# Optimization experiments

Measured on AMD Instinct MI355X. Metric: run time of the kernel, lower is better.

## Reference

```python
import jax, jax.numpy as jnp
import numpy as np

MAX_STEPS = 8
EPS = 0.1
LAM = 5.0


def setup_inputs() -> dict:
    key = jax.random.key(0)
    k1, k2, k3, k4, k5 = jax.random.split(key, 5)
    n0 = m0 = 192
    E = 191  # tree edges ~ n0 - 1
    return {
        "E1f": jax.random.randint(k1, (E, 2), 0, n0),
        "E1b": jax.random.randint(k2, (E, 2), 0, n0),
        "E2f": jax.random.randint(k3, (E, 2), 0, n0),  # unused by forward (kept for signature parity)
        "cost": jax.random.uniform(k4, (n0, m0), dtype=jnp.float32),
        "constr_f": jax.random.uniform(k5, (m0, m0), dtype=jnp.float32),
    }


def reference(E1f, E1b, E2f, cost, constr_f):
    n0, m0 = cost.shape
    S = n0 + m0
    # pad cost -> [S, S], constr_f -> [S, S] (right cols zero then bottom rows one)
    cost_p = jnp.pad(cost, ((0, m0), (0, n0)))
    cf = jnp.pad(constr_f, ((0, 0), (0, n0)))
    cf = jnp.pad(cf, ((0, n0), (0, 0)), constant_values=1.0)

    phi = cost_p.T                          # [S, S]
    phie = phi / EPS
    psi_f = (LAM * (1.0 - cf))[:, :, None]  # [S, S, 1]
    psi_b = jnp.transpose(psi_f, (1, 0, 2))

    # cdist(dst, arange(S)) == 0 indicator is exactly a one-hot of the dst index
    to_f = jax.nn.one_hot(E1f[:, 1], S, dtype=phi.dtype)  # [E, S]
    to_b = jax.nn.one_hot(E1b[:, 1], S, dtype=phi.dtype)  # [E, S]
    E = to_f.shape[0]

    def step(carry, _):
        u, v, msg_f, msg_b, sum_f, sum_b = carry
        base = sum_f + sum_b - phie
        u = jax.nn.logsumexp(base - v, axis=-2, keepdims=True)  # [1, S]
        v = jax.nn.logsumexp(base - u, axis=-1, keepdims=True)  # [S, 1]
        A = phie + u + v - sum_f - sum_b                        # [S, S]
        term_f = A @ to_f.T                                     # [S, E]
        lse_f = jax.nn.logsumexp(-(psi_f / EPS + msg_b[:, None, :]), axis=0)  # [S, E]
        msg_f = 0.5 * (msg_f + term_f + lse_f)
        sum_f = msg_f @ to_f                                    # [S, S]
        A2 = phie + u + v - sum_f - sum_b
        term_b = A2 @ to_b.T
        lse_b = jax.nn.logsumexp(-(psi_b / EPS + msg_f[:, None, :]), axis=0)
        msg_b = 0.5 * (msg_b + term_b + lse_b)
        sum_b = msg_b @ to_b
        return (u, v, msg_f, msg_b, sum_f, sum_b), None

    f32 = phi.dtype
    init = (
        jnp.zeros((1, S), f32), jnp.zeros((S, 1), f32),
        jnp.zeros((S, E), f32), jnp.zeros((S, E), f32),
        jnp.zeros((S, S), f32), jnp.zeros((S, S), f32),
    )
    (u, v, _, _, sum_f, sum_b), _ = jax.lax.scan(step, init, None, length=MAX_STEPS)

    logp = jnp.minimum(sum_f + sum_b - phie - u - v, 0.0)
    return jnp.exp(logp).T
```

## Files before the change

kernel.cpp:

```cpp
#include <hip/hip_runtime.h>
#include <math.h>

#define S      384
#define N0     192
#define NE     191
#define MAXADJ 16
#define E50    1.9287498e-22f

#define OFF_W     0
#define OFF_WT    36864
#define OFF_PHIE  73728
#define OFF_MSGF  147456
#define OFF_MSGB  221184
#define OFF_MXF   294912
#define OFF_MXB   368640
#define OFF_SBT   442368
#define OFF_BASET 516096
#define OFF_U     589824
#define OFF_V     590016
#define OFF_MAXF  590400
#define OFF_MAXB  590592
#define OFF_HIF   590784
#define OFF_LOF   590976
#define OFF_HIB   591168
#define OFF_LOB   591360
#define OFF_UHI   591552
#define OFF_INT   591616
#define IOFF_DSTF 0
#define IOFF_DSTB 192
#define IOFF_CNTF 384
#define IOFF_CNTB 576
#define IOFF_ADJF 768
#define IOFF_ADJB (768 + 192*MAXADJ)

__global__ __launch_bounds__(256) void k_setup(
    const int* __restrict__ E1f, const int* __restrict__ E1b,
    const float* __restrict__ cost, const float* __restrict__ constr,
    float* __restrict__ ws)
{
    int tid = blockIdx.x * 256 + threadIdx.x;
    int nt  = gridDim.x * 256;

    for (int idx = tid; idx < 192 * 192; idx += nt) {
        int k = idx / 192, s = idx % 192;
        float w = __expf(-50.f * (1.f - constr[idx]));
        ws[OFF_W + idx] = w;
        ws[OFF_WT + s * 192 + k] = w;
    }
    for (int idx = tid; idx < 192 * S; idx += nt) {
        int j = idx / S, i = idx % S;
        ws[OFF_PHIE + idx] = (i < N0) ? -10.f * cost[j * N0 + i] : 0.f;
        ws[OFF_MSGF + idx] = 0.f;
        ws[OFF_MSGB + idx] = 0.f;
        ws[OFF_MXF + idx]  = 0.f;
        ws[OFF_MXB + idx]  = (j < NE) ? 1.f : 0.f;
    }
    for (int i = tid; i < S; i += nt) ws[OFF_V + i] = 0.f;
    for (int i = tid; i < 192; i += nt) {
        ws[OFF_U + i] = 0.f;
        ws[OFF_MAXF + i] = 0.f; ws[OFF_MAXB + i] = 0.f;
        ws[OFF_HIF + i] = 0.f;  ws[OFF_LOF + i] = 0.f;
        ws[OFF_HIB + i] = (i < NE) ? 192.f : 0.f;
        ws[OFF_LOB + i] = (i < NE) ? 192.f : 0.f;
    }
    if (tid == 0) ws[OFF_UHI] = 0.f;

    int* ip = (int*)(ws + OFF_INT);
    for (int e = tid; e < 192; e += nt) {
        ip[IOFF_DSTF + e] = (e < NE) ? E1f[2 * e + 1] : 0;
        ip[IOFF_DSTB + e] = (e < NE) ? E1b[2 * e + 1] : 0;
    }
    for (int b = tid; b < 192; b += nt) {
        int cf = 0, cb = 0;
        for (int e = 0; e < NE; ++e) {
            if (E1f[2 * e + 1] == b && cf < MAXADJ) ip[IOFF_ADJF + b * MAXADJ + cf++] = e;
            if (E1b[2 * e + 1] == b && cb < MAXADJ) ip[IOFF_ADJB + b * MAXADJ + cb++] = e;
        }
        ip[IOFF_CNTF + b] = cf;
        ip[IOFF_CNTB + b] = cb;
    }
}

__global__ __launch_bounds__(256) void k_uv1(float* __restrict__ ws)
{
    int bid = blockIdx.x, t = threadIdx.x;
    int l = t & 63, w = t >> 6;
    const float* V = ws + OFF_V;

    if (bid == 48) {
        if (w == 0) {
            float m = -1e30f, x[6];
#pragma unroll
            for (int q = 0; q < 6; ++q) { x[q] = -V[l + 64 * q]; m = fmaxf(m, x[q]); }
#pragma unroll
            for (int o = 32; o; o >>= 1) m = fmaxf(m, __shfl_xor(m, o, 64));
            float sm = 0.f;
#pragma unroll
            for (int q = 0; q < 6; ++q) sm += __expf(x[q] - m);
#pragma unroll
            for (int o = 32; o; o >>= 1) sm += __shfl_xor(sm, o, 64);
            if (l == 0) ws[OFF_UHI] = m + __logf(sm);
        }
        return;
    }

    int j = bid * 4 + w;
    const int* ip = (const int*)(ws + OFF_INT);
    int cF = ip[IOFF_CNTF + j], cB = ip[IOFF_CNTB + j];
    const int* aF = ip + IOFF_ADJF + j * MAXADJ;
    const int* aB = ip + IOFF_ADJB + j * MAXADJ;

    float sft[6] = {0,0,0,0,0,0}, sbt[6] = {0,0,0,0,0,0};
    for (int q = 0; q < cF; ++q) {
        const float* mr = ws + OFF_MSGF + aF[q] * S;
#pragma unroll
        for (int p = 0; p < 6; ++p) sft[p] += mr[l + 64 * p];
    }
    for (int q = 0; q < cB; ++q) {
        const float* mr = ws + OFF_MSGB + aB[q] * S;
#pragma unroll
        for (int p = 0; p < 6; ++p) sbt[p] += mr[l + 64 * p];
    }

    float x[6], m = -1e30f;
#pragma unroll
    for (int p = 0; p < 6; ++p) {
        int i = l + 64 * p;
        float bt = ws[OFF_PHIE + j * S + i] + sft[p] + sbt[p];
        ws[OFF_BASET + j * S + i] = bt;
        ws[OFF_SBT + j * S + i]   = sbt[p];
        x[p] = bt - V[i];
        m = fmaxf(m, x[p]);
    }
#pragma unroll
    for (int o = 32; o; o >>= 1) m = fmaxf(m, __shfl_xor(m, o, 64));
    float sm = 0.f;
#pragma unroll
    for (int p = 0; p < 6; ++p) sm += __expf(x[p] - m);
#pragma unroll
    for (int o = 32; o; o >>= 1) sm += __shfl_xor(sm, o, 64);
    if (l == 0) ws[OFF_U + j] = m + __logf(sm);
}

__global__ __launch_bounds__(256) void k_v(float* __restrict__ ws)
{
    __shared__ float Ul[192];
    __shared__ float msh[16][17], ssh[16][17];
    int t = threadIdx.x, bid = blockIdx.x;
    if (t < 192) Ul[t] = ws[OFF_U + t];
    __syncthreads();

    const float* BT = ws + OFF_BASET;
    int il = t & 15, jg = t >> 4;
    int i = bid * 16 + il;

    float m = -1e30f, sm = 0.f;
#pragma unroll 4
    for (int j = jg; j < 192; j += 16) {
        float x = BT[j * S + i] - Ul[j];
        float mn = fmaxf(m, x);
        sm = sm * __expf(m - mn) + __expf(x - mn);
        m = mn;
    }
    msh[jg][il] = m; ssh[jg][il] = sm;
    __syncthreads();

    if (jg == 0) {
        float M = msh[0][il], Ss = ssh[0][il];
#pragma unroll
        for (int g = 1; g < 16; ++g) {
            float m2 = msh[g][il], s2 = ssh[g][il];
            float mn = fmaxf(M, m2);
            Ss = Ss * __expf(M - mn) + s2 * __expf(m2 - mn);
            M = mn;
        }
        float xt = __logf(192.f) - ws[OFF_UHI];
        float mn = fmaxf(M, xt);
        Ss = Ss * __expf(M - mn) + __expf(xt - mn);
        ws[OFF_V + i] = mn + __logf(Ss);
    }
}

__global__ __launch_bounds__(256) void k_msg(float* __restrict__ ws, int fwd)
{
    __shared__ float mx[192];
    __shared__ float red[256], red2[256];
    int e = blockIdx.x, t = threadIdx.x;
    const int* ip = (const int*)(ws + OFF_INT);

    float* MSG  = ws + (fwd ? OFF_MSGF : OFF_MSGB);
    float* MX   = ws + (fwd ? OFF_MXF  : OFF_MXB);
    const float* MXin = ws + (fwd ? OFF_MXB : OFF_MXF);
    const float* Wm   = ws + (fwd ? OFF_W   : OFF_WT);

    float mPrev = fwd ? ws[OFF_MAXB + e] : ws[OFF_MAXF + e];
    float hi    = fwd ? ws[OFF_HIB + e]  : ws[OFF_HIF + e];
    float lo    = fwd ? ws[OFF_LOB + e]  : ws[OFF_LOF + e];
    float addLo = fwd ? hi : E50 * hi;
    float yHi   = fwd ? (hi + E50 * lo) : (lo + hi);
    float lyHi  = __logf(yHi);

    int d = fwd ? ip[IOFF_DSTF + e] : ip[IOFF_DSTB + e];
    float uD = ws[OFF_U + d];
    const float* V = ws + OFF_V;

    if (t < 192) mx[t] = MXin[e * S + t];
    __syncthreads();

    float acc = 0.f;
    if (t < 192) {
#pragma unroll 8
        for (int k = 0; k < 192; ++k)
            acc += Wm[k * 192 + t] * mx[k];
    }

    int s1 = t, s2 = t + 256;
    float bt1, bt2 = 0.f;
    if (fwd) {
        bt1 = ws[OFF_BASET + d * S + s1];
        if (s2 < S) bt2 = ws[OFF_BASET + d * S + s2];
    } else {
        int cF = ip[IOFF_CNTF + d];
        const int* aF = ip + IOFF_ADJF + d * MAXADJ;
        bt1 = ws[OFF_PHIE + d * S + s1] + ws[OFF_SBT + d * S + s1];
        if (s2 < S) bt2 = ws[OFF_PHIE + d * S + s2] + ws[OFF_SBT + d * S + s2];
        for (int q = 0; q < cF; ++q) {
            const float* mr = ws + OFF_MSGF + aF[q] * S;
            bt1 += mr[s1];
            if (s2 < S) bt2 += mr[s2];
        }
    }

    float logy1 = (s1 < 192) ? __logf(acc + addLo) : lyHi;
    float x1 = 0.5f * (MSG[e * S + s1] + uD + V[s1] - bt1 + mPrev + logy1);
    float x2 = 1e30f;
    if (s2 < S) {
        x2 = 0.5f * (MSG[e * S + s2] + uD + V[s2] - bt2 + mPrev + lyHi);
        MSG[e * S + s2] = x2;
    }
    MSG[e * S + s1] = x1;

    red[t] = fminf(x1, x2);
    __syncthreads();
    for (int o = 128; o; o >>= 1) {
        if (t < o) red[t] = fminf(red[t], red[t + o]);
        __syncthreads();
    }
    float mn = red[0];
    __syncthreads();

    float mx1 = __expf(mn - x1);
    float mx2 = (s2 < S) ? __expf(mn - x2) : 0.f;
    MX[e * S + s1] = mx1;
    if (s2 < S) MX[e * S + s2] = mx2;
    if (t == 0) {
        if (fwd) ws[OFF_MAXF + e] = -mn; else ws[OFF_MAXB + e] = -mn;
    }

    red[t]  = (t < 192) ? mx1 : 0.f;
    red2[t] = ((t >= 192) ? mx1 : 0.f) + mx2;
    __syncthreads();
    for (int o = 128; o; o >>= 1) {
        if (t < o) { red[t] += red[t + o]; red2[t] += red2[t + o]; }
        __syncthreads();
    }
    if (t == 0) {
        if (fwd) { ws[OFF_LOF + e] = red[0]; ws[OFF_HIF + e] = red2[0]; }
        else     { ws[OFF_LOB + e] = red[0]; ws[OFF_HIB + e] = red2[0]; }
    }
}

__global__ __launch_bounds__(256) void k_final(const float* __restrict__ ws,
                                               float* __restrict__ out)
{
    int t = threadIdx.x;
    const int* ip = (const int*)(ws + OFF_INT);
    const float* V = ws + OFF_V;
    float uhi = ws[OFF_UHI];

    for (int a = blockIdx.x * 6; a < blockIdx.x * 6 + 6; ++a) {
        if (a < 192) {
            float ua = ws[OFF_U + a];
            int cF = ip[IOFF_CNTF + a], cB = ip[IOFF_CNTB + a];
            const int* aF = ip + IOFF_ADJF + a * MAXADJ;
            const int* aB = ip + IOFF_ADJB + a * MAXADJ;
            for (int b = t; b < S; b += 256) {
                float bt = ws[OFF_PHIE + a * S + b];
                for (int q = 0; q < cF; ++q) bt += ws[OFF_MSGF + aF[q] * S + b];
                for (int q = 0; q < cB; ++q) bt += ws[OFF_MSGB + aB[q] * S + b];
                out[a * S + b] = __expf(fminf(bt - ua - V[b], 0.f));
            }
        } else {
            for (int b = t; b < S; b += 256)
                out[a * S + b] = __expf(fminf(-uhi - V[b], 0.f));
        }
    }
}

extern "C" void kernel_launch(void* const* d_in, const int* in_sizes, int n_in,
                              void* d_out, int out_size, void* d_ws, size_t ws_size,
                              hipStream_t stream)
{
    const int*   E1f    = (const int*)d_in[0];
    const int*   E1b    = (const int*)d_in[1];
    const float* cost   = (const float*)d_in[3];
    const float* constr = (const float*)d_in[4];

    float* ws = (float*)d_ws;

    k_setup<<<64, 256, 0, stream>>>(E1f, E1b, cost, constr, ws);

    for (int step = 0; step < 8; ++step) {
        k_uv1<<<49, 256, 0, stream>>>(ws);
        k_v<<<24, 256, 0, stream>>>(ws);
        k_msg<<<NE, 256, 0, stream>>>(ws, 1);
        k_msg<<<NE, 256, 0, stream>>>(ws, 0);
    }

    k_final<<<64, 256, 0, stream>>>(ws, (float*)d_out);
}
```

Before: 250.3 us.

## Fuse all iteration kernels into one persistent cooperative kernel with counter sync

Replaces the 32 per-step kernel launches plus the final kernel with one cooperative persistent kernel of 264 blocks. Blocks take fixed roles (u rows, v columns, per-edge messages) and synchronise through global atomic counters with spin-waits instead of kernel boundaries. The aim is to remove launch and drain overhead, which dominates because each stage does very little work. The cost is relaxed atomic loads and stores at agent scope, spin-waiting, and the risk of memory-ordering bugs, since there are no explicit fences.

```diff
diff --git a/kernel.cpp b/kernel.cpp
--- a/kernel.cpp
+++ b/kernel.cpp
@@ -32,6 +32,30 @@
 #define IOFF_CNTB 576
 #define IOFF_ADJF 768
 #define IOFF_ADJB (768 + 192*MAXADJ)
+#define IOFF_SYNC (768 + 2*192*MAXADJ)
+
+#define AGT __HIP_MEMORY_SCOPE_AGENT
+
+__device__ __forceinline__ float ldc(const float* p) {
+    return __hip_atomic_load(p, __ATOMIC_RELAXED, AGT);
+}
+__device__ __forceinline__ void stc(float* p, float v) {
+    __hip_atomic_store(p, v, __ATOMIC_RELAXED, AGT);
+}
+
+__device__ __forceinline__ void arrive(unsigned* c) {
+    asm volatile("s_waitcnt vmcnt(0)" ::: "memory");
+    __syncthreads();
+    if (threadIdx.x == 0)
+        __hip_atomic_fetch_add(c, 1u, __ATOMIC_RELAXED, AGT);
+}
+__device__ __forceinline__ void wait_cnt(unsigned* c, unsigned tgt) {
+    if (threadIdx.x == 0) {
+        while (__hip_atomic_load(c, __ATOMIC_RELAXED, AGT) < tgt)
+            __builtin_amdgcn_s_sleep(2);
+    }
+    __syncthreads();
+}
 
 __global__ __launch_bounds__(256) void k_setup(
     const int* __restrict__ E1f, const int* __restrict__ E1b,
@@ -54,6 +78,8 @@
         ws[OFF_MSGB + idx] = 0.f;
         ws[OFF_MXF + idx]  = 0.f;
         ws[OFF_MXB + idx]  = (j < NE) ? 1.f : 0.f;
+        ws[OFF_SBT + idx]  = 0.f;
+        ws[OFF_BASET + idx] = 0.f;
     }
     for (int i = tid; i < S; i += nt) ws[OFF_V + i] = 0.f;
     for (int i = tid; i < 192; i += nt) {
@@ -79,220 +105,238 @@
         ip[IOFF_CNTF + b] = cf;
         ip[IOFF_CNTB + b] = cb;
     }
-}
-
-__global__ __launch_bounds__(256) void k_uv1(float* __restrict__ ws)
+    unsigned* sc = (unsigned*)(ip + IOFF_SYNC);
+    for (int i = tid; i < 32; i += nt) sc[i] = 0u;
+}
+
+__global__ __launch_bounds__(256) void k_iter(float* __restrict__ ws,
+                                              float* __restrict__ out)
 {
-    int bid = blockIdx.x, t = threadIdx.x;
-    int l = t & 63, w = t >> 6;
-    const float* V = ws + OFF_V;
-
-    if (bid == 48) {
-        if (w == 0) {
-            float m = -1e30f, x[6];
-#pragma unroll
-            for (int q = 0; q < 6; ++q) { x[q] = -V[l + 64 * q]; m = fmaxf(m, x[q]); }
-#pragma unroll
-            for (int o = 32; o; o >>= 1) m = fmaxf(m, __shfl_xor(m, o, 64));
-            float sm = 0.f;
-#pragma unroll
-            for (int q = 0; q < 6; ++q) sm += __expf(x[q] - m);
-#pragma unroll
-            for (int o = 32; o; o >>= 1) sm += __shfl_xor(sm, o, 64);
-            if (l == 0) ws[OFF_UHI] = m + __logf(sm);
+    const int bid = blockIdx.x, t = threadIdx.x;
+    const int l = t & 63, w = t >> 6;
+    int* ip = (int*)(ws + OFF_INT);
+    unsigned* sync = (unsigned*)(ip + IOFF_SYNC);
+
+    __shared__ float mx[192];
+    __shared__ float Ul[192];
+    __shared__ float red[256], red2[256];
+    __shared__ float msh[16][17], ssh[16][17];
+
+    for (int step = 0; step < 8; ++step) {
+        unsigned* sc = sync + step * 4;
+
+        if (bid < 49) {
+            if (step > 0) wait_cnt(sync + (step - 1) * 4 + 3, NE);
+            if (bid == 48) {
+                if (w == 0) {
+                    float m = -1e30f, x[6];
+#pragma unroll
+                    for (int q = 0; q < 6; ++q) {
+                        x[q] = -ldc(ws + OFF_V + l + 64 * q);
+                        m = fmaxf(m, x[q]);
+                    }
+#pragma unroll
+                    for (int o = 32; o; o >>= 1) m = fmaxf(m, __shfl_xor(m, o, 64));
+                    float sm = 0.f;
+#pragma unroll
+                    for (int q = 0; q < 6; ++q) sm += __expf(x[q] - m);
+#pragma unroll
+                    for (int o = 32; o; o >>= 1) sm += __shfl_xor(sm, o, 64);
+                    if (l == 0) stc(ws + OFF_UHI, m + __logf(sm));
+                }
+            } else {
+                int j = bid * 4 + w;
+                int cF = ip[IOFF_CNTF + j], cB = ip[IOFF_CNTB + j];
+                const int* aF = ip + IOFF_ADJF + j * MAXADJ;
+                const int* aB = ip + IOFF_ADJB + j * MAXADJ;
+
+                float sft[6] = {0,0,0,0,0,0}, sbt[6] = {0,0,0,0,0,0};
+                for (int q = 0; q < cF; ++q) {
+                    const float* mr = ws + OFF_MSGF + aF[q] * S;
+#pragma unroll
+                    for (int p = 0; p < 6; ++p) sft[p] += ldc(mr + l + 64 * p);
+                }
+                for (int q = 0; q < cB; ++q) {
+                    const float* mr = ws + OFF_MSGB + aB[q] * S;
+#pragma unroll
+                    for (int p = 0; p < 6; ++p) sbt[p] += ldc(mr + l + 64 * p);
+                }
+
+                float x[6], m = -1e30f;
+#pragma unroll
+                for (int p = 0; p < 6; ++p) {
+                    int i = l + 64 * p;
+                    float bt = ws[OFF_PHIE + j * S + i] + sft[p] + sbt[p];
+                    stc(ws + OFF_BASET + j * S + i, bt);
+                    stc(ws + OFF_SBT + j * S + i, sbt[p]);
+                    x[p] = bt - ldc(ws + OFF_V + i);
+                    m = fmaxf(m, x[p]);
+                }
+#pragma unroll
+                for (int o = 32; o; o >>= 1) m = fmaxf(m, __shfl_xor(m, o, 64));
+                float sm = 0.f;
+#pragma unroll
+                for (int p = 0; p < 6; ++p) sm += __expf(x[p] - m);
+#pragma unroll
+                for (int o = 32; o; o >>= 1) sm += __shfl_xor(sm, o, 64);
+                if (l == 0) stc(ws + OFF_U + j, m + __logf(sm));
+            }
+            arrive(&sc[0]);
+        } else if (bid < 73) {
+            wait_cnt(&sc[0], 49u);
+            if (t < 192) Ul[t] = ldc(ws + OFF_U + t);
+            __syncthreads();
+
+            int il = t & 15, jg = t >> 4;
+            int i = (bid - 49) * 16 + il;
+
+            float m = -1e30f, sm = 0.f;
+            for (int j = jg; j < 192; j += 16) {
+                float x = ldc(ws + OFF_BASET + j * S + i) - Ul[j];
+                float mn = fmaxf(m, x);
+                sm = sm * __expf(m - mn) + __expf(x - mn);
+                m = mn;
+            }
+            msh[jg][il] = m; ssh[jg][il] = sm;
+            __syncthreads();
+
+            if (jg == 0) {
+                float M = msh[0][il], Ss = ssh[0][il];
+#pragma unroll
+                for (int g = 1; g < 16; ++g) {
+                    float m2 = msh[g][il], s2 = ssh[g][il];
+                    float mn = fmaxf(M, m2);
+                    Ss = Ss * __expf(M - mn) + s2 * __expf(m2 - mn);
+                    M = mn;
+                }
+                float xt = __logf(192.f) - ldc(ws + OFF_UHI);
+                float mn = fmaxf(M, xt);
+                Ss = Ss * __expf(M - mn) + __expf(xt - mn);
+                stc(ws + OFF_V + i, mn + __logf(Ss));
+            }
+            arrive(&sc[1]);
+        } else {
+            int e = bid - 73;
+            for (int fwd = 1; fwd >= 0; --fwd) {
+                wait_cnt(fwd ? &sc[1] : &sc[2], fwd ? 24u : (unsigned)NE);
+
+                float* MSG  = ws + (fwd ? OFF_MSGF : OFF_MSGB);
+                float* MX   = ws + (fwd ? OFF_MXF  : OFF_MXB);
+                const float* MXin = ws + (fwd ? OFF_MXB : OFF_MXF);
+                const float* Wm   = ws + (fwd ? OFF_W   : OFF_WT);
+
+                float mPrev = fwd ? ws[OFF_MAXB + e] : ws[OFF_MAXF + e];
+                float hi    = fwd ? ws[OFF_HIB + e]  : ws[OFF_HIF + e];
+                float lo    = fwd ? ws[OFF_LOB + e]  : ws[OFF_LOF + e];
+                float addLo = fwd ? hi : E50 * hi;
+                float yHi   = fwd ? (hi + E50 * lo) : (lo + hi);
+                float lyHi  = __logf(yHi);
+
+                int d = fwd ? ip[IOFF_DSTF + e] : ip[IOFF_DSTB + e];
+                float uD = ldc(ws + OFF_U + d);
+
+                if (t < 192) mx[t] = MXin[e * S + t];
+                __syncthreads();
+
+                float acc = 0.f;
+                if (t < 192) {
+#pragma unroll 8
+                    for (int k = 0; k < 192; ++k)
+                        acc += Wm[k * 192 + t] * mx[k];
+                }
+
+                int s1 = t, s2 = t + 256;
+                float bt1, bt2 = 0.f;
+                if (fwd) {
+                    bt1 = ldc(ws + OFF_BASET + d * S + s1);
+                    if (s2 < S) bt2 = ldc(ws + OFF_BASET + d * S + s2);
+                } else {
+                    int cF = ip[IOFF_CNTF + d];
+                    const int* aF = ip + IOFF_ADJF + d * MAXADJ;
+                    bt1 = ws[OFF_PHIE + d * S + s1] + ldc(ws + OFF_SBT + d * S + s1);
+                    if (s2 < S)
+                        bt2 = ws[OFF_PHIE + d * S + s2] + ldc(ws + OFF_SBT + d * S + s2);
+                    for (int q = 0; q < cF; ++q) {
+                        const float* mr = ws + OFF_MSGF + aF[q] * S;
+                        bt1 += ldc(mr + s1);
+                        if (s2 < S) bt2 += ldc(mr + s2);
+                    }
+                }
+
+                float v1 = ldc(ws + OFF_V + s1);
+                float v2 = (s2 < S) ? ldc(ws + OFF_V + s2) : 0.f;
+
+                float logy1 = (s1 < 192) ? __logf(acc + addLo) : lyHi;
+                float x1 = 0.5f * (ldc(MSG + e * S + s1) + uD + v1 - bt1 + mPrev + logy1);
+                float x2 = 1e30f;
+                if (s2 < S) {
+                    x2 = 0.5f * (ldc(MSG + e * S + s2) + uD + v2 - bt2 + mPrev + lyHi);
+                    stc(MSG + e * S + s2, x2);
+                }
+                stc(MSG + e * S + s1, x1);
+
+                red[t] = fminf(x1, x2);
+                __syncthreads();
+                for (int o = 128; o; o >>= 1) {
+                    if (t < o) red[t] = fminf(red[t], red[t + o]);
+                    __syncthreads();
+                }
+                float mn = red[0];
+                __syncthreads();
+
+                float mx1 = __expf(mn - x1);
+                float mx2 = (s2 < S) ? __expf(mn - x2) : 0.f;
+                MX[e * S + s1] = mx1;
+                if (s2 < S) MX[e * S + s2] = mx2;
+                if (t == 0) {
+                    if (fwd) ws[OFF_MAXF + e] = -mn; else ws[OFF_MAXB + e] = -mn;
+                }
+
+                red[t]  = (t < 192) ? mx1 : 0.f;
+                red2[t] = ((t >= 192) ? mx1 : 0.f) + mx2;
+                __syncthreads();
+                for (int o = 128; o; o >>= 1) {
+                    if (t < o) { red[t] += red[t + o]; red2[t] += red2[t + o]; }
+                    __syncthreads();
+                }
+                if (t == 0) {
+                    if (fwd) { ws[OFF_LOF + e] = red[0]; ws[OFF_HIF + e] = red2[0]; }
+                    else     { ws[OFF_LOB + e] = red[0]; ws[OFF_HIB + e] = red2[0]; }
+                }
+                __syncthreads();
+                arrive(fwd ? &sc[2] : &sc[3]);
+            }
         }
-        return;
-    }
-
-    int j = bid * 4 + w;
-    const int* ip = (const int*)(ws + OFF_INT);
-    int cF = ip[IOFF_CNTF + j], cB = ip[IOFF_CNTB + j];
-    const int* aF = ip + IOFF_ADJF + j * MAXADJ;
-    const int* aB = ip + IOFF_ADJB + j * MAXADJ;
-
-    float sft[6] = {0,0,0,0,0,0}, sbt[6] = {0,0,0,0,0,0};
-    for (int q = 0; q < cF; ++q) {
-        const float* mr = ws + OFF_MSGF + aF[q] * S;
-#pragma unroll
-        for (int p = 0; p < 6; ++p) sft[p] += mr[l + 64 * p];
-    }
-    for (int q = 0; q < cB; ++q) {
-        const float* mr = ws + OFF_MSGB + aB[q] * S;
-#pragma unroll
-        for (int p = 0; p < 6; ++p) sbt[p] += mr[l + 64 * p];
-    }
-
-    float x[6], m = -1e30f;
-#pragma unroll
-    for (int p = 0; p < 6; ++p) {
-        int i = l + 64 * p;
-        float bt = ws[OFF_PHIE + j * S + i] + sft[p] + sbt[p];
-        ws[OFF_BASET + j * S + i] = bt;
-        ws[OFF_SBT + j * S + i]   = sbt[p];
-        x[p] = bt - V[i];
-        m = fmaxf(m, x[p]);
-    }
-#pragma unroll
-    for (int o = 32; o; o >>= 1) m = fmaxf(m, __shfl_xor(m, o, 64));
-    float sm = 0.f;
-#pragma unroll
-    for (int p = 0; p < 6; ++p) sm += __expf(x[p] - m);
-#pragma unroll
-    for (int o = 32; o; o >>= 1) sm += __shfl_xor(sm, o, 64);
-    if (l == 0) ws[OFF_U + j] = m + __logf(sm);
-}
-
-__global__ __launch_bounds__(256) void k_v(float* __restrict__ ws)
-{
-    __shared__ float Ul[192];
-    __shared__ float msh[16][17], ssh[16][17];
-    int t = threadIdx.x, bid = blockIdx.x;
-    if (t < 192) Ul[t] = ws[OFF_U + t];
-    __syncthreads();
-
-    const float* BT = ws + OFF_BASET;
-    int il = t & 15, jg = t >> 4;
-    int i = bid * 16 + il;
-
-    float m = -1e30f, sm = 0.f;
-#pragma unroll 4
-    for (int j = jg; j < 192; j += 16) {
-        float x = BT[j * S + i] - Ul[j];
-        float mn = fmaxf(m, x);
-        sm = sm * __expf(m - mn) + __expf(x - mn);
-        m = mn;
-    }
-    msh[jg][il] = m; ssh[jg][il] = sm;
-    __syncthreads();
-
-    if (jg == 0) {
-        float M = msh[0][il], Ss = ssh[0][il];
-#pragma unroll
-        for (int g = 1; g < 16; ++g) {
-            float m2 = msh[g][il], s2 = ssh[g][il];
-            float mn = fmaxf(M, m2);
-            Ss = Ss * __expf(M - mn) + s2 * __expf(m2 - mn);
-            M = mn;
-        }
-        float xt = __logf(192.f) - ws[OFF_UHI];
-        float mn = fmaxf(M, xt);
-        Ss = Ss * __expf(M - mn) + __expf(xt - mn);
-        ws[OFF_V + i] = mn + __logf(Ss);
-    }
-}
-
-__global__ __launch_bounds__(256) void k_msg(float* __restrict__ ws, int fwd)
-{
-    __shared__ float mx[192];
-    __shared__ float red[256], red2[256];
-    int e = blockIdx.x, t = threadIdx.x;
-    const int* ip = (const int*)(ws + OFF_INT);
-
-    float* MSG  = ws + (fwd ? OFF_MSGF : OFF_MSGB);
-    float* MX   = ws + (fwd ? OFF_MXF  : OFF_MXB);
-    const float* MXin = ws + (fwd ? OFF_MXB : OFF_MXF);
-    const float* Wm   = ws + (fwd ? OFF_W   : OFF_WT);
-
-    float mPrev = fwd ? ws[OFF_MAXB + e] : ws[OFF_MAXF + e];
-    float hi    = fwd ? ws[OFF_HIB + e]  : ws[OFF_HIF + e];
-    float lo    = fwd ? ws[OFF_LOB + e]  : ws[OFF_LOF + e];
-    float addLo = fwd ? hi : E50 * hi;
-    float yHi   = fwd ? (hi + E50 * lo) : (lo + hi);
-    float lyHi  = __logf(yHi);
-
-    int d = fwd ? ip[IOFF_DSTF + e] : ip[IOFF_DSTB + e];
-    float uD = ws[OFF_U + d];
-    const float* V = ws + OFF_V;
-
-    if (t < 192) mx[t] = MXin[e * S + t];
-    __syncthreads();
-
-    float acc = 0.f;
-    if (t < 192) {
-#pragma unroll 8
-        for (int k = 0; k < 192; ++k)
-            acc += Wm[k * 192 + t] * mx[k];
-    }
-
-    int s1 = t, s2 = t + 256;
-    float bt1, bt2 = 0.f;
-    if (fwd) {
-        bt1 = ws[OFF_BASET + d * S + s1];
-        if (s2 < S) bt2 = ws[OFF_BASET + d * S + s2];
-    } else {
-        int cF = ip[IOFF_CNTF + d];
-        const int* aF = ip + IOFF_ADJF + d * MAXADJ;
-        bt1 = ws[OFF_PHIE + d * S + s1] + ws[OFF_SBT + d * S + s1];
-        if (s2 < S) bt2 = ws[OFF_PHIE + d * S + s2] + ws[OFF_SBT + d * S + s2];
-        for (int q = 0; q < cF; ++q) {
-            const float* mr = ws + OFF_MSGF + aF[q] * S;
-            bt1 += mr[s1];
-            if (s2 < S) bt2 += mr[s2];
-        }
-    }
-
-    float logy1 = (s1 < 192) ? __logf(acc + addLo) : lyHi;
-    float x1 = 0.5f * (MSG[e * S + s1] + uD + V[s1] - bt1 + mPrev + logy1);
-    float x2 = 1e30f;
-    if (s2 < S) {
-        x2 = 0.5f * (MSG[e * S + s2] + uD + V[s2] - bt2 + mPrev + lyHi);
-        MSG[e * S + s2] = x2;
-    }
-    MSG[e * S + s1] = x1;
-
-    red[t] = fminf(x1, x2);
-    __syncthreads();
-    for (int o = 128; o; o >>= 1) {
-        if (t < o) red[t] = fminf(red[t], red[t + o]);
-        __syncthreads();
-    }
-    float mn = red[0];
-    __syncthreads();
-
-    float mx1 = __expf(mn - x1);
-    float mx2 = (s2 < S) ? __expf(mn - x2) : 0.f;
-    MX[e * S + s1] = mx1;
-    if (s2 < S) MX[e * S + s2] = mx2;
-    if (t == 0) {
-        if (fwd) ws[OFF_MAXF + e] = -mn; else ws[OFF_MAXB + e] = -mn;
-    }
-
-    red[t]  = (t < 192) ? mx1 : 0.f;
-    red2[t] = ((t >= 192) ? mx1 : 0.f) + mx2;
-    __syncthreads();
-    for (int o = 128; o; o >>= 1) {
-        if (t < o) { red[t] += red[t + o]; red2[t] += red2[t + o]; }
-        __syncthreads();
-    }
-    if (t == 0) {
-        if (fwd) { ws[OFF_LOF + e] = red[0]; ws[OFF_HIF + e] = red2[0]; }
-        else     { ws[OFF_LOB + e] = red[0]; ws[OFF_HIB + e] = red2[0]; }
-    }
-}
-
-__global__ __launch_bounds__(256) void k_final(const float* __restrict__ ws,
-                                               float* __restrict__ out)
-{
-    int t = threadIdx.x;
-    const int* ip = (const int*)(ws + OFF_INT);
-    const float* V = ws + OFF_V;
-    float uhi = ws[OFF_UHI];
-
-    for (int a = blockIdx.x * 6; a < blockIdx.x * 6 + 6; ++a) {
+    }
+
+    wait_cnt(sync + 7 * 4 + 3, NE);
+    float uhi = ldc(ws + OFF_UHI);
+    for (int a = bid; a < S; a += 264) {
+        int s1 = t, s2 = t + 256;
+        float v1 = ldc(ws + OFF_V + s1);
+        float v2 = (s2 < S) ? ldc(ws + OFF_V + s2) : 0.f;
         if (a < 192) {
-            float ua = ws[OFF_U + a];
+            float ua = ldc(ws + OFF_U + a);
             int cF = ip[IOFF_CNTF + a], cB = ip[IOFF_CNTB + a];
             const int* aF = ip + IOFF_ADJF + a * MAXADJ;
             const int* aB = ip + IOFF_ADJB + a * MAXADJ;
-            for (int b = t; b < S; b += 256) {
-                float bt = ws[OFF_PHIE + a * S + b];
-                for (int q = 0; q < cF; ++q) bt += ws[OFF_MSGF + aF[q] * S + b];
-                for (int q = 0; q < cB; ++q) bt += ws[OFF_MSGB + aB[q] * S + b];
-                out[a * S + b] = __expf(fminf(bt - ua - V[b], 0.f));
-            }
+            float bt1 = ws[OFF_PHIE + a * S + s1];
+            float bt2 = (s2 < S) ? ws[OFF_PHIE + a * S + s2] : 0.f;
+            for (int q = 0; q < cF; ++q) {
+                const float* mr = ws + OFF_MSGF + aF[q] * S;
+                bt1 += ldc(mr + s1);
+                if (s2 < S) bt2 += ldc(mr + s2);
+            }
+            for (int q = 0; q < cB; ++q) {
+                const float* mr = ws + OFF_MSGB + aB[q] * S;
+                bt1 += ldc(mr + s1);
+                if (s2 < S) bt2 += ldc(mr + s2);
+            }
+            out[a * S + s1] = __expf(fminf(bt1 - ua - v1, 0.f));
+            if (s2 < S) out[a * S + s2] = __expf(fminf(bt2 - ua - v2, 0.f));
         } else {
-            for (int b = t; b < S; b += 256)
-                out[a * S + b] = __expf(fminf(-uhi - V[b], 0.f));
+            out[a * S + s1] = __expf(fminf(-uhi - v1, 0.f));
+            if (s2 < S) out[a * S + s2] = __expf(fminf(-uhi - v2, 0.f));
         }
     }
 }
@@ -306,16 +350,12 @@
     const float* cost   = (const float*)d_in[3];
     const float* constr = (const float*)d_in[4];
 
-    float* ws = (float*)d_ws;
+    float* ws   = (float*)d_ws;
+    float* outp = (float*)d_out;
 
     k_setup<<<64, 256, 0, stream>>>(E1f, E1b, cost, constr, ws);
 
-    for (int step = 0; step < 8; ++step) {
-        k_uv1<<<49, 256, 0, stream>>>(ws);
-        k_v<<<24, 256, 0, stream>>>(ws);
-        k_msg<<<NE, 256, 0, stream>>>(ws, 1);
-        k_msg<<<NE, 256, 0, stream>>>(ws, 0);
-    }
-
-    k_final<<<64, 256, 0, stream>>>(ws, (float*)d_out);
-}
+    void* args[] = { (void*)&ws, (void*)&outp };
+    hipLaunchCooperativeKernel((const void*)k_iter, dim3(264), dim3(256),
+                               args, 0, stream);
+}
```

Result: slower. 434.9 us (+73.7%).

## Fuse u and v logsumexp kernels into a single-block kernel

Applied to the files above, without the earlier changes.

Merges the u-update kernel (49 blocks) and the v-update kernel (24 blocks) into one 1024-thread single-block kernel that computes u, stores it in shared memory, and then computes v after a block barrier. This removes one kernel launch and its global synchronization per step. In exchange, all the work runs on one CU: each wave handles 12 rows serially and the v reduction splits into two halves. That could make the step slower than the multi-block version if launch overhead was not the dominant cost.

```diff
diff --git a/kernel.cpp b/kernel.cpp
--- a/kernel.cpp
+++ b/kernel.cpp
@@ -81,103 +81,107 @@
     }
 }
 
-__global__ __launch_bounds__(256) void k_uv1(float* __restrict__ ws)
-{
-    int bid = blockIdx.x, t = threadIdx.x;
+__global__ __launch_bounds__(1024) void k_ab(float* __restrict__ ws)
+{
+    __shared__ float uS[192];
+    __shared__ float vP[384];
+    __shared__ float pm[768], pssum[768];
+    __shared__ float uhiS;
+
+    int t = threadIdx.x;
     int l = t & 63, w = t >> 6;
-    const float* V = ws + OFF_V;
-
-    if (bid == 48) {
-        if (w == 0) {
-            float m = -1e30f, x[6];
-#pragma unroll
-            for (int q = 0; q < 6; ++q) { x[q] = -V[l + 64 * q]; m = fmaxf(m, x[q]); }
-#pragma unroll
-            for (int o = 32; o; o >>= 1) m = fmaxf(m, __shfl_xor(m, o, 64));
-            float sm = 0.f;
-#pragma unroll
-            for (int q = 0; q < 6; ++q) sm += __expf(x[q] - m);
-#pragma unroll
-            for (int o = 32; o; o >>= 1) sm += __shfl_xor(sm, o, 64);
-            if (l == 0) ws[OFF_UHI] = m + __logf(sm);
-        }
-        return;
-    }
-
-    int j = bid * 4 + w;
     const int* ip = (const int*)(ws + OFF_INT);
-    int cF = ip[IOFF_CNTF + j], cB = ip[IOFF_CNTB + j];
-    const int* aF = ip + IOFF_ADJF + j * MAXADJ;
-    const int* aB = ip + IOFF_ADJB + j * MAXADJ;
-
-    float sft[6] = {0,0,0,0,0,0}, sbt[6] = {0,0,0,0,0,0};
-    for (int q = 0; q < cF; ++q) {
-        const float* mr = ws + OFF_MSGF + aF[q] * S;
-#pragma unroll
-        for (int p = 0; p < 6; ++p) sft[p] += mr[l + 64 * p];
-    }
-    for (int q = 0; q < cB; ++q) {
-        const float* mr = ws + OFF_MSGB + aB[q] * S;
-#pragma unroll
-        for (int p = 0; p < 6; ++p) sbt[p] += mr[l + 64 * p];
-    }
-
-    float x[6], m = -1e30f;
-#pragma unroll
-    for (int p = 0; p < 6; ++p) {
-        int i = l + 64 * p;
-        float bt = ws[OFF_PHIE + j * S + i] + sft[p] + sbt[p];
-        ws[OFF_BASET + j * S + i] = bt;
-        ws[OFF_SBT + j * S + i]   = sbt[p];
-        x[p] = bt - V[i];
-        m = fmaxf(m, x[p]);
-    }
-#pragma unroll
-    for (int o = 32; o; o >>= 1) m = fmaxf(m, __shfl_xor(m, o, 64));
-    float sm = 0.f;
-#pragma unroll
-    for (int p = 0; p < 6; ++p) sm += __expf(x[p] - m);
-#pragma unroll
-    for (int o = 32; o; o >>= 1) sm += __shfl_xor(sm, o, 64);
-    if (l == 0) ws[OFF_U + j] = m + __logf(sm);
-}
-
-__global__ __launch_bounds__(256) void k_v(float* __restrict__ ws)
-{
-    __shared__ float Ul[192];
-    __shared__ float msh[16][17], ssh[16][17];
-    int t = threadIdx.x, bid = blockIdx.x;
-    if (t < 192) Ul[t] = ws[OFF_U + t];
-    __syncthreads();
-
-    const float* BT = ws + OFF_BASET;
-    int il = t & 15, jg = t >> 4;
-    int i = bid * 16 + il;
-
-    float m = -1e30f, sm = 0.f;
+
+    if (t < 384) vP[t] = ws[OFF_V + t];
+    __syncthreads();
+
+    for (int r = 0; r < 12; ++r) {
+        int j = w * 12 + r;
+        int cF = ip[IOFF_CNTF + j], cB = ip[IOFF_CNTB + j];
+        const int* aF = ip + IOFF_ADJF + j * MAXADJ;
+        const int* aB = ip + IOFF_ADJB + j * MAXADJ;
+
+        float sft[6] = {0,0,0,0,0,0}, sbt[6] = {0,0,0,0,0,0};
+        for (int q = 0; q < cF; ++q) {
+            const float* mr = ws + OFF_MSGF + aF[q] * S;
+#pragma unroll
+            for (int p = 0; p < 6; ++p) sft[p] += mr[l + 64 * p];
+        }
+        for (int q = 0; q < cB; ++q) {
+            const float* mr = ws + OFF_MSGB + aB[q] * S;
+#pragma unroll
+            for (int p = 0; p < 6; ++p) sbt[p] += mr[l + 64 * p];
+        }
+
+        float x[6], m = -1e30f;
+#pragma unroll
+        for (int p = 0; p < 6; ++p) {
+            int i = l + 64 * p;
+            float bt = ws[OFF_PHIE + j * S + i] + sft[p] + sbt[p];
+            ws[OFF_BASET + j * S + i] = bt;
+            ws[OFF_SBT + j * S + i]   = sbt[p];
+            x[p] = bt - vP[i];
+            m = fmaxf(m, x[p]);
+        }
+#pragma unroll
+        for (int o = 32; o; o >>= 1) m = fmaxf(m, __shfl_xor(m, o, 64));
+        float sm = 0.f;
+#pragma unroll
+        for (int p = 0; p < 6; ++p) sm += __expf(x[p] - m);
+#pragma unroll
+        for (int o = 32; o; o >>= 1) sm += __shfl_xor(sm, o, 64);
+        if (l == 0) {
+            float uj = m + __logf(sm);
+            ws[OFF_U + j] = uj;
+            uS[j] = uj;
+        }
+    }
+
+    if (w == 0) {
+        float x[6], m = -1e30f;
+#pragma unroll
+        for (int q = 0; q < 6; ++q) { x[q] = -vP[l + 64 * q]; m = fmaxf(m, x[q]); }
+#pragma unroll
+        for (int o = 32; o; o >>= 1) m = fmaxf(m, __shfl_xor(m, o, 64));
+        float sm = 0.f;
+#pragma unroll
+        for (int q = 0; q < 6; ++q) sm += __expf(x[q] - m);
+#pragma unroll
+        for (int o = 32; o; o >>= 1) sm += __shfl_xor(sm, o, 64);
+        if (l == 0) {
+            float uh = m + __logf(sm);
+            uhiS = uh;
+            ws[OFF_UHI] = uh;
+        }
+    }
+    __threadfence_block();
+    __syncthreads();
+
+    if (t < 768) {
+        int half = t / 384, i = t - half * 384;
+        float m = -1e30f, sm = 0.f;
+        int j0 = half * 96;
 #pragma unroll 4
-    for (int j = jg; j < 192; j += 16) {
-        float x = BT[j * S + i] - Ul[j];
-        float mn = fmaxf(m, x);
-        sm = sm * __expf(m - mn) + __expf(x - mn);
-        m = mn;
-    }
-    msh[jg][il] = m; ssh[jg][il] = sm;
-    __syncthreads();
-
-    if (jg == 0) {
-        float M = msh[0][il], Ss = ssh[0][il];
-#pragma unroll
-        for (int g = 1; g < 16; ++g) {
-            float m2 = msh[g][il], s2 = ssh[g][il];
-            float mn = fmaxf(M, m2);
-            Ss = Ss * __expf(M - mn) + s2 * __expf(m2 - mn);
-            M = mn;
-        }
-        float xt = __logf(192.f) - ws[OFF_UHI];
-        float mn = fmaxf(M, xt);
+        for (int j = j0; j < j0 + 96; ++j) {
+            float x = ws[OFF_BASET + j * S + i] - uS[j];
+            float mn = fmaxf(m, x);
+            sm = sm * __expf(m - mn) + __expf(x - mn);
+            m = mn;
+        }
+        pm[half * 384 + i] = m;
+        pssum[half * 384 + i] = sm;
+    }
+    __syncthreads();
+    if (t < 384) {
+        float M = pm[t], Ss = pssum[t];
+        float m2 = pm[384 + t], s2 = pssum[384 + t];
+        float mn = fmaxf(M, m2);
+        Ss = Ss * __expf(M - mn) + s2 * __expf(m2 - mn);
+        M = mn;
+        float xt = __logf(192.f) - uhiS;
+        mn = fmaxf(M, xt);
         Ss = Ss * __expf(M - mn) + __expf(xt - mn);
-        ws[OFF_V + i] = mn + __logf(Ss);
+        ws[OFF_V + t] = mn + __logf(Ss);
     }
 }
 
@@ -311,8 +315,7 @@
     k_setup<<<64, 256, 0, stream>>>(E1f, E1b, cost, constr, ws);
 
     for (int step = 0; step < 8; ++step) {
-        k_uv1<<<49, 256, 0, stream>>>(ws);
-        k_v<<<24, 256, 0, stream>>>(ws);
+        k_ab<<<1, 1024, 0, stream>>>(ws);
         k_msg<<<NE, 256, 0, stream>>>(ws, 1);
         k_msg<<<NE, 256, 0, stream>>>(ws, 0);
     }
```

Measured after the change: 524.6 us. 2.1x slower.
